# Performance work log

Hardware: AMD Instinct MI355X
Metric: run time of the kernel (lower is better)

The kernel has to match this reference:

```python
import jax, jax.numpy as jnp
import numpy as np

B, T, C_FEAT, H = 1024, 256, 512, 256


def setup_inputs() -> dict:
    key = jax.random.key(0)
    ks = jax.random.split(key, 8)
    s_ih = 1.0 / np.sqrt(H)
    return {
        "features": jax.random.normal(ks[0], (B, T, C_FEAT), dtype=jnp.float32),
        "last_coord": jax.random.normal(ks[1], (B, 2), dtype=jnp.float32),
        "W_ih": jax.random.uniform(ks[2], (3 * H, C_FEAT + 2), jnp.float32, -s_ih, s_ih),
        "W_hh": jax.random.uniform(ks[3], (3 * H, H), jnp.float32, -s_ih, s_ih),
        "b_ih": jax.random.uniform(ks[4], (3 * H,), jnp.float32, -s_ih, s_ih),
        "b_hh": jax.random.uniform(ks[5], (3 * H,), jnp.float32, -s_ih, s_ih),
        "W_proj": jax.random.uniform(ks[6], (2, H), jnp.float32, -s_ih, s_ih),
        "b_proj": jax.random.uniform(ks[7], (2,), jnp.float32, -s_ih, s_ih),
    }


def reference(features, last_coord, W_ih, W_hh, b_ih, b_hh, W_proj, b_proj):
    # features: (B, T, C_feat); last_coord: (B, 2)
    Bb, Tt, Cf = features.shape
    Hh = W_hh.shape[1]
    h0 = jnp.zeros((Bb, Hh), dtype=features.dtype)

    def step(carry, feat_t):
        h, coord = carry
        x = jnp.concatenate([feat_t, coord], axis=1)          # (B, C+2)
        gi = x @ W_ih.T + b_ih                                 # (B, 3H)
        gh = h @ W_hh.T + b_hh                                 # (B, 3H)
        i_r, i_z, i_n = jnp.split(gi, 3, axis=1)
        h_r, h_z, h_n = jnp.split(gh, 3, axis=1)
        r = jax.nn.sigmoid(i_r + h_r)
        z = jax.nn.sigmoid(i_z + h_z)
        n = jnp.tanh(i_n + r * h_n)
        h_new = (1.0 - z) * n + z * h                          # PyTorch GRU update
        disp = h_new @ W_proj.T + b_proj                       # (B, 2)
        return (h_new, coord + disp), disp

    feats_t = jnp.swapaxes(features, 0, 1)                     # (T, B, C)
    _, disps = jax.lax.scan(step, (h0, last_coord), feats_t)   # (T, B, 2)
    return jnp.swapaxes(disps, 0, 1)                           # (B, T, 2)
```

## Files before the change

### kernel.cpp

```cpp
#include <hip/hip_runtime.h>
#include <stdint.h>

typedef unsigned short u16;
typedef unsigned int   u32;
typedef __attribute__((ext_vector_type(8))) __bf16 bf16x8;
typedef __attribute__((ext_vector_type(4))) float  f32x4;
typedef __attribute__((ext_vector_type(8))) u16    u16x8;
typedef __attribute__((ext_vector_type(4))) u16    u16x4;
typedef __attribute__((ext_vector_type(2))) u32    u32x2;

__device__ __forceinline__ u16 f2bf(float f) {
    u32 u = __float_as_uint(f);
    u32 r = (u + 0x7fffu + ((u >> 16) & 1u)) >> 16;
    return (u16)r;
}
__device__ __forceinline__ float bf2f(u16 v) { return __uint_as_float(((u32)v) << 16); }
__device__ __forceinline__ bf16x8 as_bf(u16x8 x) { union { u16x8 a; bf16x8 b; } u; u.a = x; return u.b; }
__device__ __forceinline__ void gload_lds16(const void* g, void* l) {
    __builtin_amdgcn_global_load_lds((const __attribute__((address_space(1))) void*)g,
                                     (__attribute__((address_space(3))) void*)l, 16, 0, 0);
}

__global__ void k_prep(const float* __restrict__ W_ih, const float* __restrict__ W_hh,
                       const float* __restrict__ b_ih, const float* __restrict__ b_hh,
                       u16* __restrict__ Wf, u16* __restrict__ Whh, float* __restrict__ bsum) {
    int i = blockIdx.x * 256 + threadIdx.x;
    if (i < 768 * 512) { int o = i >> 9, k = i & 511; Wf[i] = f2bf(W_ih[o * 514 + k]); }
    if (i < 768 * 256) { Whh[i] = f2bf(W_hh[i]); }
    if (i < 768)       { bsum[i] = b_ih[i] + (i < 512 ? b_hh[i] : 0.f); }
}

__global__ void k_cast(const float* __restrict__ f, u16* __restrict__ o) {
    const size_t N8 = (size_t)262144 * 512 / 8;
    for (size_t i = (size_t)blockIdx.x * 256 + threadIdx.x; i < N8; i += (size_t)gridDim.x * 256) {
        float4 a = ((const float4*)f)[i * 2];
        float4 b = ((const float4*)f)[i * 2 + 1];
        u16x8 v;
        v[0] = f2bf(a.x); v[1] = f2bf(a.y); v[2] = f2bf(a.z); v[3] = f2bf(a.w);
        v[4] = f2bf(b.x); v[5] = f2bf(b.y); v[6] = f2bf(b.z); v[7] = f2bf(b.w);
        ((u16x8*)o)[i] = v;
    }
}

__global__ __launch_bounds__(256) void k_gemm(const u16* __restrict__ featbf,
                                              const u16* __restrict__ Wf,
                                              const float* __restrict__ bsum,
                                              float* __restrict__ Gf) {
    __shared__ u16 As[128 * 64];
    __shared__ u16 Bs[128 * 64];
    const int tid = threadIdx.x;
    const int l = tid & 63, wv = tid >> 6;
    const int wr = wv >> 1, wc = wv & 1;
    const int lb = l & 15, lq = l >> 4;
    const int n0 = blockIdx.x * 128;
    const int m0 = blockIdx.y * 128;
    const int rl = l >> 3;
    const int c16 = (l & 7) * 16;
    const int sswz = (rl & 7) << 4;

    f32x4 acc[4][4] = {};

    for (int k0 = 0; k0 < 512; k0 += 64) {
        __syncthreads();
#pragma unroll
        for (int i = 0; i < 4; ++i) {
            int ci = wv * 4 + i;
            int r = ci * 8 + rl;
            const char* sa = (const char*)(featbf + (size_t)(m0 + r) * 512) + k0 * 2 + (c16 ^ sswz);
            gload_lds16(sa, (char*)As + ci * 1024);
            const char* sb = (const char*)(Wf + (size_t)(n0 + r) * 512) + k0 * 2 + (c16 ^ sswz);
            gload_lds16(sb, (char*)Bs + ci * 1024);
        }
        __syncthreads();
#pragma unroll
        for (int kc = 0; kc < 2; ++kc) {
            bf16x8 af[4], bfr[4];
#pragma unroll
            for (int mi = 0; mi < 4; ++mi) {
                int row = wr * 64 + mi * 16 + lb;
                af[mi] = *(const bf16x8*)((char*)As + row * 128 + (((kc * 32 + lq * 8) * 2) ^ ((row & 7) << 4)));
            }
#pragma unroll
            for (int ni = 0; ni < 4; ++ni) {
                int row = wc * 64 + ni * 16 + lb;
                bfr[ni] = *(const bf16x8*)((char*)Bs + row * 128 + (((kc * 32 + lq * 8) * 2) ^ ((row & 7) << 4)));
            }
#pragma unroll
            for (int mi = 0; mi < 4; ++mi)
#pragma unroll
                for (int ni = 0; ni < 4; ++ni)
                    acc[mi][ni] = __builtin_amdgcn_mfma_f32_16x16x32_bf16(af[mi], bfr[ni], acc[mi][ni], 0, 0, 0);
        }
    }
#pragma unroll
    for (int ni = 0; ni < 4; ++ni) {
        int o = n0 + wc * 64 + ni * 16 + lb;
        float bi = bsum[o];
#pragma unroll
        for (int mi = 0; mi < 4; ++mi) {
#pragma unroll
            for (int j = 0; j < 4; ++j) {
                int m = m0 + wr * 64 + mi * 16 + lq * 4 + j;
                int bb = m >> 8, tt = m & 255;
                Gf[(size_t)((tt << 10) + bb) * 768 + o] = acc[mi][ni][j] + bi;
            }
        }
    }
}

template<typename ST>
__global__ __launch_bounds__(256) void k_gemm_legacy(const float* __restrict__ feat,
                                                     const u16* __restrict__ Wf,
                                                     const float* __restrict__ bsum,
                                                     ST* __restrict__ Gf) {
    __shared__ u16 As[128 * 64];
    __shared__ u16 Bs[128 * 64];
    const int tid = threadIdx.x;
    const int l = tid & 63, wv = tid >> 6;
    const int wr = wv >> 1, wc = wv & 1;
    const int lb = l & 15, lq = l >> 4;
    const int n0 = blockIdx.x * 128;
    const int m0 = blockIdx.y * 128;
    const int srow = tid >> 1, scol = (tid & 1) * 32;

    f32x4 acc[4][4] = {};

    for (int k0 = 0; k0 < 512; k0 += 64) {
        __syncthreads();
        const float* ga = feat + (size_t)(m0 + srow) * 512 + k0 + scol;
        const u16*   gb = Wf + (n0 + srow) * 512 + k0 + scol;
        char* arow = (char*)As + srow * 128;
        char* brow = (char*)Bs + srow * 128;
        const int swz = (srow & 7) << 4;
#pragma unroll
        for (int i = 0; i < 4; ++i) {
            float4 f0 = *(const float4*)(ga + i * 8);
            float4 f1 = *(const float4*)(ga + i * 8 + 4);
            u16x8 v;
            v[0] = f2bf(f0.x); v[1] = f2bf(f0.y); v[2] = f2bf(f0.z); v[3] = f2bf(f0.w);
            v[4] = f2bf(f1.x); v[5] = f2bf(f1.y); v[6] = f2bf(f1.z); v[7] = f2bf(f1.w);
            *(u16x8*)(arow + (((scol + i * 8) * 2) ^ swz)) = v;
            u16x8 w8 = *(const u16x8*)(gb + i * 8);
            *(u16x8*)(brow + (((scol + i * 8) * 2) ^ swz)) = w8;
        }
        __syncthreads();
#pragma unroll
        for (int kc = 0; kc < 2; ++kc) {
            bf16x8 af[4], bfr[4];
#pragma unroll
            for (int mi = 0; mi < 4; ++mi) {
                int row = wr * 64 + mi * 16 + lb;
                af[mi] = *(const bf16x8*)((char*)As + row * 128 + (((kc * 32 + lq * 8) * 2) ^ ((row & 7) << 4)));
            }
#pragma unroll
            for (int ni = 0; ni < 4; ++ni) {
                int row = wc * 64 + ni * 16 + lb;
                bfr[ni] = *(const bf16x8*)((char*)Bs + row * 128 + (((kc * 32 + lq * 8) * 2) ^ ((row & 7) << 4)));
            }
#pragma unroll
            for (int mi = 0; mi < 4; ++mi)
#pragma unroll
                for (int ni = 0; ni < 4; ++ni)
                    acc[mi][ni] = __builtin_amdgcn_mfma_f32_16x16x32_bf16(af[mi], bfr[ni], acc[mi][ni], 0, 0, 0);
        }
    }
#pragma unroll
    for (int ni = 0; ni < 4; ++ni) {
        int o = n0 + wc * 64 + ni * 16 + lb;
        float bi = bsum[o];
#pragma unroll
        for (int mi = 0; mi < 4; ++mi) {
#pragma unroll
            for (int j = 0; j < 4; ++j) {
                int m = m0 + wr * 64 + mi * 16 + lq * 4 + j;
                int bb = m >> 8, tt = m & 255;
                size_t idx = (size_t)((tt << 10) + bb) * 768 + o;
                float v = acc[mi][ni][j] + bi;
                if constexpr (sizeof(ST) == 4) Gf[idx] = v; else Gf[idx] = f2bf(v);
            }
        }
    }
}

template<typename ST>
__global__ __launch_bounds__(512, 2) void k_rnn(const float* __restrict__ lastc,
                                                const float* __restrict__ W_ih,
                                                const float* __restrict__ bhh_g,
                                                const float* __restrict__ Wp,
                                                const float* __restrict__ bp,
                                                const u16* __restrict__ Whh,
                                                const ST* __restrict__ Gf,
                                                float* __restrict__ out) {
    __shared__ u16 Wlds[3 * 768 * 32];
    __shared__ u16 hbf[16 * 320];
    __shared__ float wpL[256 * 2];
    __shared__ float coordL[16 * 2];
    __shared__ float dPart[8 * 16 * 2];

    const int tid = threadIdx.x, l = tid & 63, wv = tid >> 6;
    const int lb = l & 15, lq = l >> 4;
    const int bb = blockIdx.x << 4;
    const int swz = (lb & 7) << 4;

    bf16x8 wres[5][3][2];
    bf16x8 wcf[3][2];
    float bhhn[2][4];
#pragma unroll
    for (int g = 0; g < 3; ++g)
#pragma unroll
        for (int ut = 0; ut < 2; ++ut) {
            int row = g * 256 + (2 * wv + ut) * 16 + lb;
#pragma unroll
            for (int kc = 0; kc < 5; ++kc)
                wres[kc][g][ut] = *(const bf16x8*)(Whh + row * 256 + kc * 32 + lq * 8);
            u16x8 cf = {0, 0, 0, 0, 0, 0, 0, 0};
            if (lq == 0) {
                cf[0] = f2bf(W_ih[row * 514 + 512]);
                cf[1] = f2bf(W_ih[row * 514 + 513]);
            }
            wcf[g][ut] = as_bf(cf);
        }
#pragma unroll
    for (int ut = 0; ut < 2; ++ut)
#pragma unroll
        for (int j = 0; j < 4; ++j)
            bhhn[ut][j] = bhh_g[512 + (2 * wv + ut) * 16 + lq * 4 + j];

    for (int i = tid; i < 3 * 768 * 16; i += 512) {
        int kcs = i / (768 * 16), rem = i - kcs * (768 * 16);
        int row = rem >> 4, kh = rem & 15;
        ((u32*)Wlds)[i] = *(const u32*)(Whh + row * 256 + (5 + kcs) * 32 + kh * 2);
    }
    for (int i = tid; i < 16 * 320 / 2; i += 512) ((u32*)hbf)[i] = 0u;
    if (tid < 256) { wpL[tid * 2] = Wp[tid]; wpL[tid * 2 + 1] = Wp[256 + tid]; }
    float bpc = (tid < 32) ? bp[tid & 1] : 0.f;
    __syncthreads();
    if (tid < 32) {
        int b = tid >> 1, c = tid & 1;
        float cc = lastc[(bb + b) * 2 + c];
        coordL[b * 2 + c] = cc;
        *(u16*)((char*)hbf + b * 640 + 512 + ((c * 2) ^ ((b & 7) << 4))) = f2bf(cc);
    }
    __syncthreads();

    float hreg[2][4] = {};
    const ST* gr = Gf + (size_t)(bb + lb) * 768 + lq * 4;
    const char* hrow = (const char*)hbf + lb * 640;

    for (int t = 0; t < 256; ++t) {
        float gf[3][2][4];
#pragma unroll
        for (int g = 0; g < 3; ++g)
#pragma unroll
            for (int ut = 0; ut < 2; ++ut) {
                int off = g * 256 + (2 * wv + ut) * 16;
                if constexpr (sizeof(ST) == 4) {
                    float4 v = *(const float4*)(gr + off);
                    gf[g][ut][0] = v.x; gf[g][ut][1] = v.y; gf[g][ut][2] = v.z; gf[g][ut][3] = v.w;
                } else {
                    u16x4 v = *(const u16x4*)(gr + off);
#pragma unroll
                    for (int j = 0; j < 4; ++j) gf[g][ut][j] = bf2f(v[j]);
                }
            }

        f32x4 acc[3][2] = {};
        f32x4 accC[2] = {};
#pragma unroll
        for (int kc = 0; kc < 5; ++kc) {
            bf16x8 hb = *(const bf16x8*)(hrow + ((kc * 64 + lq * 16) ^ swz));
#pragma unroll
            for (int g = 0; g < 3; ++g)
#pragma unroll
                for (int ut = 0; ut < 2; ++ut)
                    acc[g][ut] = __builtin_amdgcn_mfma_f32_16x16x32_bf16(wres[kc][g][ut], hb, acc[g][ut], 0, 0, 0);
        }
#pragma unroll
        for (int kcs = 0; kcs < 3; ++kcs) {
            bf16x8 hb = *(const bf16x8*)(hrow + (((5 + kcs) * 64 + lq * 16) ^ swz));
#pragma unroll
            for (int g = 0; g < 3; ++g)
#pragma unroll
                for (int ut = 0; ut < 2; ++ut) {
                    int row = g * 256 + (2 * wv + ut) * 16 + lb;
                    bf16x8 wl = *(const bf16x8*)((const char*)Wlds + (size_t)(kcs * 768 + row) * 64 + lq * 16);
                    acc[g][ut] = __builtin_amdgcn_mfma_f32_16x16x32_bf16(wl, hb, acc[g][ut], 0, 0, 0);
                }
        }
        {
            bf16x8 hbE = *(const bf16x8*)(hrow + 512 + ((lq * 16) ^ swz));
#pragma unroll
            for (int ut = 0; ut < 2; ++ut) {
                acc[0][ut] = __builtin_amdgcn_mfma_f32_16x16x32_bf16(wcf[0][ut], hbE, acc[0][ut], 0, 0, 0);
                acc[1][ut] = __builtin_amdgcn_mfma_f32_16x16x32_bf16(wcf[1][ut], hbE, acc[1][ut], 0, 0, 0);
                accC[ut]   = __builtin_amdgcn_mfma_f32_16x16x32_bf16(wcf[2][ut], hbE, accC[ut],   0, 0, 0);
            }
        }
        __syncthreads();

        float pd0 = 0.f, pd1 = 0.f;
#pragma unroll
        for (int ut = 0; ut < 2; ++ut) {
            int ub = (2 * wv + ut) * 16 + lq * 4;
            float4 wpa = *(const float4*)(wpL + ub * 2);
            float4 wpb = *(const float4*)(wpL + ub * 2 + 4);
            u16 hpk[4];
#pragma unroll
            for (int j = 0; j < 4; ++j) {
                float r = 1.f / (1.f + __expf(-(gf[0][ut][j] + acc[0][ut][j])));
                float z = 1.f / (1.f + __expf(-(gf[1][ut][j] + acc[1][ut][j])));
                float ghn = acc[2][ut][j] + bhhn[ut][j];
                float xn = gf[2][ut][j] + accC[ut][j] + r * ghn;
                float e = __expf(-2.f * fabsf(xn));
                float th = (1.f - e) / (1.f + e);
                th = (xn >= 0.f) ? th : -th;
                float hn = (1.f - z) * th + z * hreg[ut][j];
                hreg[ut][j] = hn;
                float w0 = (j == 0) ? wpa.x : (j == 1) ? wpa.z : (j == 2) ? wpb.x : wpb.z;
                float w1 = (j == 0) ? wpa.y : (j == 1) ? wpa.w : (j == 2) ? wpb.y : wpb.w;
                pd0 += w0 * hn;
                pd1 += w1 * hn;
                hpk[j] = f2bf(hn);
            }
            u32x2 pv;
            pv.x = (u32)hpk[0] | ((u32)hpk[1] << 16);
            pv.y = (u32)hpk[2] | ((u32)hpk[3] << 16);
            *(u32x2*)((char*)hbf + lb * 640 + ((ub * 2) ^ swz)) = pv;
        }
        pd0 += __shfl_xor(pd0, 16); pd0 += __shfl_xor(pd0, 32);
        pd1 += __shfl_xor(pd1, 16); pd1 += __shfl_xor(pd1, 32);
        if (l < 16) { dPart[(wv * 16 + l) * 2] = pd0; dPart[(wv * 16 + l) * 2 + 1] = pd1; }
        __syncthreads();

        if (tid < 32) {
            int b = tid >> 1, c = tid & 1;
            float d = bpc;
#pragma unroll
            for (int w8 = 0; w8 < 8; ++w8) d += dPart[(w8 * 16 + b) * 2 + c];
            out[((size_t)(bb + b) * 256 + t) * 2 + c] = d;
            float nc = coordL[b * 2 + c] + d;
            coordL[b * 2 + c] = nc;
            *(u16*)((char*)hbf + b * 640 + 512 + ((c * 2) ^ ((b & 7) << 4))) = f2bf(nc);
        }
        __syncthreads();
        gr += (size_t)1024 * 768;
    }
}

extern "C" void kernel_launch(void* const* d_in, const int* in_sizes, int n_in,
                              void* d_out, int out_size, void* d_ws, size_t ws_size,
                              hipStream_t stream) {
    const float* feat   = (const float*)d_in[0];
    const float* lastc  = (const float*)d_in[1];
    const float* W_ih   = (const float*)d_in[2];
    const float* W_hh   = (const float*)d_in[3];
    const float* b_ih   = (const float*)d_in[4];
    const float* b_hh   = (const float*)d_in[5];
    const float* W_proj = (const float*)d_in[6];
    const float* b_proj = (const float*)d_in[7];
    float* out = (float*)d_out;

    char* ws = (char*)d_ws;
    u16*   Wf    = (u16*)ws;
    u16*   Whh   = (u16*)(ws + 786432);
    float* bsum  = (float*)(ws + 786432 + 393216);
    const size_t off_fb = 786432 + 393216 + 3072;
    u16*   featbf = (u16*)(ws + off_fb);
    const size_t off_gf_full = off_fb + (size_t)262144 * 512 * 2;
    const size_t need_full  = off_gf_full + (size_t)262144 * 768 * 4;
    const size_t need_tier2 = off_fb + (size_t)262144 * 768 * 4;
    const size_t need_tier3 = off_fb + (size_t)262144 * 768 * 2;

    k_prep<<<1536, 256, 0, stream>>>(W_ih, W_hh, b_ih, b_hh, Wf, Whh, bsum);

    if (ws_size >= need_full) {
        float* Gf = (float*)(ws + off_gf_full);
        k_cast<<<16384, 256, 0, stream>>>(feat, featbf);
        k_gemm<<<dim3(6, 2048), 256, 0, stream>>>(featbf, Wf, bsum, Gf);
        k_rnn<float><<<64, 512, 0, stream>>>(lastc, W_ih, b_hh, W_proj, b_proj, Whh, Gf, out);
    } else if (ws_size >= need_tier2) {
        float* Gf = (float*)(ws + off_fb);
        k_gemm_legacy<float><<<dim3(6, 2048), 256, 0, stream>>>(feat, Wf, bsum, Gf);
        k_rnn<float><<<64, 512, 0, stream>>>(lastc, W_ih, b_hh, W_proj, b_proj, Whh, Gf, out);
    } else {
        u16* Gf = (u16*)(ws + off_fb);
        (void)need_tier3;
        k_gemm_legacy<u16><<<dim3(6, 2048), 256, 0, stream>>>(feat, Wf, bsum, Gf);
        k_rnn<u16><<<64, 512, 0, stream>>>(lastc, W_ih, b_hh, W_proj, b_proj, Whh, Gf, out);
    }
}
```

Baseline: 1.482 ms.

## Double-buffer RNN hidden state, rebalance register/LDS weights, remap GEMM blocks per XCD

The recurrent kernel now keeps the bf16 hidden state in two LDS buffers that alternate by step parity, which removes one of the two block barriers per timestep. It holds six K-chunks of W_hh in registers instead of five, moving the rest into a smaller LDS area laid out per lane so each read is contiguous. The GEMM kernels remap block indices so that consecutive logical tiles land on the same XCD, aiming for better L2 reuse. The cost is more register pressure in the RNN kernel, which could cause spills at 512 threads with two blocks per CU.

```diff
diff --git a/kernel.cpp b/kernel.cpp
--- a/kernel.cpp
+++ b/kernel.cpp
@@ -40,6 +40,13 @@
         v[4] = f2bf(b.x); v[5] = f2bf(b.y); v[6] = f2bf(b.z); v[7] = f2bf(b.w);
         ((u16x8*)o)[i] = v;
     }
+}
+
+__device__ __forceinline__ void xcd_remap(int& n0, int& m0) {
+    int phys = blockIdx.x + blockIdx.y * 6;
+    int logical = (phys & 7) * 1536 + (phys >> 3);
+    n0 = (logical % 6) * 128;
+    m0 = (logical / 6) * 128;
 }
 
 __global__ __launch_bounds__(256) void k_gemm(const u16* __restrict__ featbf,
@@ -52,8 +59,7 @@
     const int l = tid & 63, wv = tid >> 6;
     const int wr = wv >> 1, wc = wv & 1;
     const int lb = l & 15, lq = l >> 4;
-    const int n0 = blockIdx.x * 128;
-    const int m0 = blockIdx.y * 128;
+    int n0, m0; xcd_remap(n0, m0);
     const int rl = l >> 3;
     const int c16 = (l & 7) * 16;
     const int sswz = (rl & 7) << 4;
@@ -119,8 +125,7 @@
     const int l = tid & 63, wv = tid >> 6;
     const int wr = wv >> 1, wc = wv & 1;
     const int lb = l & 15, lq = l >> 4;
-    const int n0 = blockIdx.x * 128;
-    const int m0 = blockIdx.y * 128;
+    int n0, m0; xcd_remap(n0, m0);
     const int srow = tid >> 1, scol = (tid & 1) * 32;
 
     f32x4 acc[4][4] = {};
@@ -191,8 +196,8 @@
                                                 const u16* __restrict__ Whh,
                                                 const ST* __restrict__ Gf,
                                                 float* __restrict__ out) {
-    __shared__ u16 Wlds[3 * 768 * 32];
-    __shared__ u16 hbf[16 * 320];
+    __shared__ u16 Wlds[96 * 512];
+    __shared__ u16 hbf[2][16 * 320];
     __shared__ float wpL[256 * 2];
     __shared__ float coordL[16 * 2];
     __shared__ float dPart[8 * 16 * 2];
@@ -202,7 +207,7 @@
     const int bb = blockIdx.x << 4;
     const int swz = (lb & 7) << 4;
 
-    bf16x8 wres[5][3][2];
+    bf16x8 wres[6][3][2];
     bf16x8 wcf[3][2];
     float bhhn[2][4];
 #pragma unroll
@@ -211,7 +216,7 @@
         for (int ut = 0; ut < 2; ++ut) {
             int row = g * 256 + (2 * wv + ut) * 16 + lb;
 #pragma unroll
-            for (int kc = 0; kc < 5; ++kc)
+            for (int kc = 0; kc < 6; ++kc)
                 wres[kc][g][ut] = *(const bf16x8*)(Whh + row * 256 + kc * 32 + lq * 8);
             u16x8 cf = {0, 0, 0, 0, 0, 0, 0, 0};
             if (lq == 0) {
@@ -226,12 +231,14 @@
         for (int j = 0; j < 4; ++j)
             bhhn[ut][j] = bhh_g[512 + (2 * wv + ut) * 16 + lq * 4 + j];
 
-    for (int i = tid; i < 3 * 768 * 16; i += 512) {
-        int kcs = i / (768 * 16), rem = i - kcs * (768 * 16);
-        int row = rem >> 4, kh = rem & 15;
-        ((u32*)Wlds)[i] = *(const u32*)(Whh + row * 256 + (5 + kcs) * 32 + kh * 2);
-    }
-    for (int i = tid; i < 16 * 320 / 2; i += 512) ((u32*)hbf)[i] = 0u;
+    for (int i = tid; i < 24576; i += 512) {
+        int s = i >> 8, r = i & 255, ll = r >> 2, e = r & 3;
+        int g = s >> 5, rem = s & 31, tt = rem >> 1, kcs = rem & 1;
+        int row = g * 256 + tt * 16 + (ll & 15);
+        int k = (6 + kcs) * 32 + (ll >> 4) * 8 + e * 2;
+        ((u32*)Wlds)[i] = *(const u32*)(Whh + row * 256 + k);
+    }
+    for (int i = tid; i < 2 * 16 * 320 / 2; i += 512) ((u32*)hbf)[i] = 0u;
     if (tid < 256) { wpL[tid * 2] = Wp[tid]; wpL[tid * 2 + 1] = Wp[256 + tid]; }
     float bpc = (tid < 32) ? bp[tid & 1] : 0.f;
     __syncthreads();
@@ -245,7 +252,7 @@
 
     float hreg[2][4] = {};
     const ST* gr = Gf + (size_t)(bb + lb) * 768 + lq * 4;
-    const char* hrow = (const char*)hbf + lb * 640;
+    int par = 0;
 
     for (int t = 0; t < 256; ++t) {
         float gf[3][2][4];
@@ -264,10 +271,11 @@
                 }
             }
 
+        const char* hrow = (const char*)hbf + par * 10240 + lb * 640;
         f32x4 acc[3][2] = {};
         f32x4 accC[2] = {};
 #pragma unroll
-        for (int kc = 0; kc < 5; ++kc) {
+        for (int kc = 0; kc < 6; ++kc) {
             bf16x8 hb = *(const bf16x8*)(hrow + ((kc * 64 + lq * 16) ^ swz));
 #pragma unroll
             for (int g = 0; g < 3; ++g)
@@ -276,14 +284,14 @@
                     acc[g][ut] = __builtin_amdgcn_mfma_f32_16x16x32_bf16(wres[kc][g][ut], hb, acc[g][ut], 0, 0, 0);
         }
 #pragma unroll
-        for (int kcs = 0; kcs < 3; ++kcs) {
-            bf16x8 hb = *(const bf16x8*)(hrow + (((5 + kcs) * 64 + lq * 16) ^ swz));
+        for (int kcs = 0; kcs < 2; ++kcs) {
+            bf16x8 hb = *(const bf16x8*)(hrow + (((6 + kcs) * 64 + lq * 16) ^ swz));
 #pragma unroll
             for (int g = 0; g < 3; ++g)
 #pragma unroll
                 for (int ut = 0; ut < 2; ++ut) {
-                    int row = g * 256 + (2 * wv + ut) * 16 + lb;
-                    bf16x8 wl = *(const bf16x8*)((const char*)Wlds + (size_t)(kcs * 768 + row) * 64 + lq * 16);
+                    int s = (g * 16 + (2 * wv + ut)) * 2 + kcs;
+                    bf16x8 wl = *(const bf16x8*)((const char*)Wlds + s * 1024 + l * 16);
                     acc[g][ut] = __builtin_amdgcn_mfma_f32_16x16x32_bf16(wl, hb, acc[g][ut], 0, 0, 0);
                 }
         }
@@ -296,8 +304,8 @@
                 accC[ut]   = __builtin_amdgcn_mfma_f32_16x16x32_bf16(wcf[2][ut], hbE, accC[ut],   0, 0, 0);
             }
         }
-        __syncthreads();
-
+
+        char* hwr = (char*)hbf + (par ^ 1) * 10240 + lb * 640;
         float pd0 = 0.f, pd1 = 0.f;
 #pragma unroll
         for (int ut = 0; ut < 2; ++ut) {
@@ -325,7 +333,7 @@
             u32x2 pv;
             pv.x = (u32)hpk[0] | ((u32)hpk[1] << 16);
             pv.y = (u32)hpk[2] | ((u32)hpk[3] << 16);
-            *(u32x2*)((char*)hbf + lb * 640 + ((ub * 2) ^ swz)) = pv;
+            *(u32x2*)(hwr + ((ub * 2) ^ swz)) = pv;
         }
         pd0 += __shfl_xor(pd0, 16); pd0 += __shfl_xor(pd0, 32);
         pd1 += __shfl_xor(pd1, 16); pd1 += __shfl_xor(pd1, 32);
@@ -340,9 +348,10 @@
             out[((size_t)(bb + b) * 256 + t) * 2 + c] = d;
             float nc = coordL[b * 2 + c] + d;
             coordL[b * 2 + c] = nc;
-            *(u16*)((char*)hbf + b * 640 + 512 + ((c * 2) ^ ((b & 7) << 4))) = f2bf(nc);
-        }
-        __syncthreads();
+            *(u16*)((char*)hbf + (par ^ 1) * 10240 + b * 640 + 512 + ((c * 2) ^ ((b & 7) << 4))) = f2bf(nc);
+        }
+        __syncthreads();
+        par ^= 1;
         gr += (size_t)1024 * 768;
     }
 }
@@ -369,7 +378,6 @@
     const size_t off_gf_full = off_fb + (size_t)262144 * 512 * 2;
     const size_t need_full  = off_gf_full + (size_t)262144 * 768 * 4;
     const size_t need_tier2 = off_fb + (size_t)262144 * 768 * 4;
-    const size_t need_tier3 = off_fb + (size_t)262144 * 768 * 2;
 
     k_prep<<<1536, 256, 0, stream>>>(W_ih, W_hh, b_ih, b_hh, Wf, Whh, bsum);
 
@@ -384,7 +392,6 @@
         k_rnn<float><<<64, 512, 0, stream>>>(lastc, W_ih, b_hh, W_proj, b_proj, Whh, Gf, out);
     } else {
         u16* Gf = (u16*)(ws + off_fb);
-        (void)need_tier3;
         k_gemm_legacy<u16><<<dim3(6, 2048), 256, 0, stream>>>(feat, Wf, bsum, Gf);
         k_rnn<u16><<<64, 512, 0, stream>>>(lastc, W_ih, b_hh, W_proj, b_proj, Whh, Gf, out);
     }
```

Result: slower. 1.531 ms (+3.3%).
